# Optimization experiments

Measured on AMD Instinct MI355X. Metric: run time of the kernel, lower is better.

Reference implementation:

```python
import jax, jax.numpy as jnp
import numpy as np

N_LAYERS = 5
EMB = 300
G = 2048
L_SEM = 10
V_SEM = 30
NUM_TASKS = 128
TAU = 1.0
GUM_TAU = 1.0
BN_EPS = 1e-5


def _bn(x, g, b):
    # training-mode batch norm (biased variance over batch dim)
    m = jnp.mean(x, 0)
    v = jnp.var(x, 0)
    return (x - m) / jnp.sqrt(v + BN_EPS) * g + b


def setup_inputs() -> dict:
    key = jax.random.key(0)
    ks = iter(jax.random.split(key, 64))
    N, E = 100000, 400000
    s = 0.02
    inp = {}
    inp['x_idx'] = jax.random.randint(next(ks), (N,), 0, 119)
    inp['edge_index'] = jax.random.randint(next(ks), (2, E), 0, N)
    inp['edge_attr'] = jax.random.randint(next(ks), (E,), 0, 5)
    inp['batch'] = jnp.sort(jax.random.randint(next(ks), (N,), 0, G))
    u = jax.random.uniform(next(ks), (G, L_SEM, V_SEM), minval=1e-8, maxval=1.0)
    inp['gumbel'] = -jnp.log(-jnp.log(u))  # standard Gumbel(0,1) noise
    nrm = lambda shape: jax.random.normal(next(ks), shape, dtype=jnp.float32) * s
    inp['atom_emb'] = nrm((119, EMB))
    inp['bond_emb'] = nrm((N_LAYERS, 5, EMB))
    inp['eps'] = jnp.zeros((N_LAYERS,), jnp.float32)
    inp['gin_W1'] = nrm((N_LAYERS, EMB, 2 * EMB)); inp['gin_b1'] = jnp.zeros((N_LAYERS, 2 * EMB))
    inp['gin_bn1_g'] = jnp.ones((N_LAYERS, 2 * EMB)); inp['gin_bn1_b'] = jnp.zeros((N_LAYERS, 2 * EMB))
    inp['gin_W2'] = nrm((N_LAYERS, 2 * EMB, EMB)); inp['gin_b2'] = jnp.zeros((N_LAYERS, EMB))
    inp['node_bn_g'] = jnp.ones((N_LAYERS, EMB)); inp['node_bn_b'] = jnp.zeros((N_LAYERS, EMB))
    M = N_LAYERS - 1
    inp['vn_W1'] = nrm((M, EMB, 2 * EMB)); inp['vn_b1'] = jnp.zeros((M, 2 * EMB))
    inp['vn_bn1_g'] = jnp.ones((M, 2 * EMB)); inp['vn_bn1_b'] = jnp.zeros((M, 2 * EMB))
    inp['vn_W2'] = nrm((M, 2 * EMB, EMB)); inp['vn_b2'] = jnp.zeros((M, EMB))
    inp['vn_bn2_g'] = jnp.ones((M, EMB)); inp['vn_bn2_b'] = jnp.zeros((M, EMB))
    inp['pre_W'] = nrm((EMB, L_SEM * V_SEM)); inp['pre_b'] = jnp.zeros((L_SEM * V_SEM,))
    inp['sel_W'] = nrm((V_SEM, 3)); inp['sel_b'] = jnp.zeros((3,))
    inp['aft_W'] = nrm((3 * L_SEM, EMB)); inp['aft_b'] = jnp.zeros((EMB,))
    inp['hW1'] = nrm((EMB, 128)); inp['hb1'] = jnp.zeros((128,))
    inp['hW2'] = nrm((128, 128)); inp['hb2'] = jnp.zeros((128,))
    inp['hW3'] = nrm((128, NUM_TASKS)); inp['hb3'] = jnp.zeros((NUM_TASKS,))
    return inp


def reference(x_idx, edge_index, edge_attr, batch, gumbel,
              atom_emb, bond_emb, eps,
              gin_W1, gin_b1, gin_bn1_g, gin_bn1_b, gin_W2, gin_b2,
              node_bn_g, node_bn_b,
              vn_W1, vn_b1, vn_bn1_g, vn_bn1_b, vn_W2, vn_b2, vn_bn2_g, vn_bn2_b,
              pre_W, pre_b, sel_W, sel_b, aft_W, aft_b,
              hW1, hb1, hW2, hb2, hW3, hb3):
    N = x_idx.shape[0]
    src, dst = edge_index[0], edge_index[1]
    h = atom_emb[x_idx]                               # [N, EMB]
    vn = jnp.zeros((G, EMB), h.dtype)                 # virtual node starts at zero embedding
    for l in range(N_LAYERS):
        hl = h + vn[batch]
        # GINConv: aggregate relu(x_src + bond_emb) onto dst, then MLP((1+eps)x + aggr)
        msg = jax.nn.relu(hl[src] + bond_emb[l][edge_attr])   # [E, EMB]
        agg = jax.ops.segment_sum(msg, dst, num_segments=N)
        t = (1.0 + eps[l]) * hl + agg
        t = jax.nn.relu(_bn(t @ gin_W1[l] + gin_b1[l], gin_bn1_g[l], gin_bn1_b[l]))
        t = t @ gin_W2[l] + gin_b2[l]
        t = _bn(t, node_bn_g[l], node_bn_b[l])
        if l < N_LAYERS - 1:
            t = jax.nn.relu(t)
            # virtual node update (dropout omitted: eval mode)
            vtmp = jax.ops.segment_sum(hl, batch, num_segments=G) + vn
            v1 = jax.nn.relu(_bn(vtmp @ vn_W1[l] + vn_b1[l], vn_bn1_g[l], vn_bn1_b[l]))
            vn = jax.nn.relu(_bn(v1 @ vn_W2[l] + vn_b2[l], vn_bn2_g[l], vn_bn2_b[l]))
        h = t
    # global mean pool
    cnt = jnp.maximum(jax.ops.segment_sum(jnp.ones((N,), h.dtype), batch, num_segments=G), 1.0)
    h_graph = jax.ops.segment_sum(h, batch, num_segments=G) / cnt[:, None]
    # SEM head: gumbel-softmax (hard, straight-through)
    logits = ((h_graph @ pre_W + pre_b) / TAU).reshape(G, L_SEM, V_SEM)
    y = (logits + gumbel) / GUM_TAU
    y_soft = jax.nn.softmax(y, axis=-1)
    y_hard = jax.nn.one_hot(jnp.argmax(y, axis=-1), V_SEM, dtype=y_soft.dtype)
    oht = jax.lax.stop_gradient(y_hard - y_soft) + y_soft
    msg_w = oht @ sel_W + sel_b                        # [G, L, 3]
    dis = msg_w.reshape(G, 3 * L_SEM) @ aft_W + aft_b  # [G, EMB]
    o = jax.nn.relu(dis @ hW1 + hb1)
    o = jax.nn.relu(o @ hW2 + hb2)
    return o @ hW3 + hb3                               # [G, num_tasks]
```

## Files before the change

### kernel.cpp

```cpp
#include <hip/hip_runtime.h>
#include <cstdint>

#define EMBD 300
#define GNUM 2048
#define LSEM 10
#define VSEM 30
#define NLAY 5
#define GRAM_KB 24

typedef __attribute__((ext_vector_type(8))) short short8v;
typedef __attribute__((ext_vector_type(4))) float f32x4;

__device__ __forceinline__ void split3(float x, short& h1, short& h2, short& h3) {
  unsigned u = __float_as_uint(x);
  unsigned uh = (u + 0x7FFFu + ((u >> 16) & 1u)) & 0xFFFF0000u;
  h1 = (short)(uh >> 16);
  float r = x - __uint_as_float(uh);
  unsigned v = __float_as_uint(r);
  unsigned vh = (v + 0x7FFFu + ((v >> 16) & 1u)) & 0xFFFF0000u;
  h2 = (short)(vh >> 16);
  float r2 = r - __uint_as_float(vh);
  unsigned w = __float_as_uint(r2);
  unsigned wh = (w + 0x7FFFu + ((w >> 16) & 1u)) & 0xFFFF0000u;
  h3 = (short)(wh >> 16);
}

__device__ __forceinline__ unsigned cvt_pk_bf16(float lo, float hi) {
  unsigned r;
  asm("v_cvt_pk_bf16_f32 %0, %1, %2" : "=v"(r) : "v"(lo), "v"(hi));
  return r;
}

__device__ __forceinline__ void split3_pair(float x0, float x1,
                                            unsigned& u1, unsigned& u2, unsigned& u3) {
  u1 = cvt_pk_bf16(x0, x1);
  float r0 = x0 - __uint_as_float(u1 << 16);
  float r1 = x1 - __uint_as_float(u1 & 0xFFFF0000u);
  u2 = cvt_pk_bf16(r0, r1);
  float s0 = r0 - __uint_as_float(u2 << 16);
  float s1 = r1 - __uint_as_float(u2 & 0xFFFF0000u);
  u3 = cvt_pk_bf16(s0, s1);
}

__global__ void k_diag(float* __restrict__ p, int n, float v) {
  int i = blockIdx.x * blockDim.x + threadIdx.x;
  if (i < n) p[i] = v;
}

__global__ void k_zero(float* __restrict__ p, int n) {
  int i = blockIdx.x * blockDim.x + threadIdx.x;
  if (i < n) p[i] = 0.f;
}

__global__ void k_seti(int* __restrict__ p, int n, int v) {
  int i = blockIdx.x * blockDim.x + threadIdx.x;
  if (i < n) p[i] = v;
}

__global__ void k_offsets(const int* __restrict__ batch, int N, int* __restrict__ off) {
  int g = blockIdx.x * blockDim.x + threadIdx.x;
  if (g > GNUM) return;
  int lo = 0, hi = N;
  while (lo < hi) { int mid = (lo + hi) >> 1; if (batch[mid] < g) lo = mid + 1; else hi = mid; }
  off[g] = lo;
}

__global__ void k_deg(const int* __restrict__ dst, int E, int* __restrict__ deg) {
  int e = blockIdx.x * blockDim.x + threadIdx.x;
  if (e < E) atomicAdd(&deg[dst[e]], 1);
}

__global__ void k_scan1(const int* __restrict__ deg, int N,
                        int* __restrict__ incl, int* __restrict__ part) {
  __shared__ int s[256];
  int tid = threadIdx.x;
  int i = blockIdx.x * 256 + tid;
  int v = (i < N) ? deg[i] : 0;
  s[tid] = v; __syncthreads();
  for (int o = 1; o < 256; o <<= 1) {
    int t = (tid >= o) ? s[tid - o] : 0;
    __syncthreads();
    s[tid] += t;
    __syncthreads();
  }
  if (i < N) incl[i] = s[tid];
  if (tid == 255) part[blockIdx.x] = s[255];
}

__global__ void k_scan2(int* __restrict__ part, int nb) {
  __shared__ int s[512];
  int t = threadIdx.x;
  if (nb <= 512) {
    int v = (t < nb) ? part[t] : 0;
    s[t] = v; __syncthreads();
    for (int o = 1; o < 512; o <<= 1) {
      int u = (t >= o) ? s[t - o] : 0;
      __syncthreads();
      s[t] += u;
      __syncthreads();
    }
    if (t < nb) part[t] = s[t] - v;
  } else if (t == 0) {
    int run = 0;
    for (int i = 0; i < nb; i++) { int x = part[i]; part[i] = run; run += x; }
  }
}

__global__ void k_scan3(const int* __restrict__ deg, const int* __restrict__ incl,
                        const int* __restrict__ part, int N, int E, int* __restrict__ off2) {
  int i = blockIdx.x * blockDim.x + threadIdx.x;
  if (i < N) off2[i] = part[i >> 8] + incl[i] - deg[i];
  if (i == 0) off2[N] = E;
}

__global__ void k_copyi(const int* __restrict__ a, int* __restrict__ b, int n) {
  int i = blockIdx.x * blockDim.x + threadIdx.x;
  if (i < n) b[i] = a[i];
}

__global__ void k_fill(const int* __restrict__ dst, int E,
                       int* __restrict__ cur, int* __restrict__ eix) {
  int e = blockIdx.x * blockDim.x + threadIdx.x;
  if (e >= E) return;
  int p = atomicAdd(&cur[dst[e]], 1);
  eix[p] = e;
}

template<bool FIRST>
__global__ void k_hl(const float* __restrict__ aemb, const int* __restrict__ x_idx,
                     const float* __restrict__ scale, const float* __restrict__ shift,
                     const int* __restrict__ batch, const float* __restrict__ vn,
                     const float* __restrict__ epsArr, int l,
                     float* pt, float* __restrict__ hl, int N)
{
  int i = blockIdx.x;
  int c = threadIdx.x;
  if (c >= EMBD) return;
  float x;
  if (FIRST) {
    x = aemb[(size_t)x_idx[i] * EMBD + c];
  } else {
    x = pt[(size_t)i * EMBD + c];
    x = fmaxf(fmaf(x, scale[c], shift[c]), 0.f);
  }
  float h = x + vn[(size_t)batch[i] * EMBD + c];
  hl[(size_t)i * EMBD + c] = h;
  pt[(size_t)i * EMBD + c] = (1.f + epsArr[l]) * h;
}

__global__ void k_gather(const int* __restrict__ off2, const int* __restrict__ eix,
                         const int* __restrict__ src, const int* __restrict__ eattr,
                         const float* __restrict__ hl, const float* __restrict__ bond,
                         float* __restrict__ tacc, int N)
{
  int node = blockIdx.x * 4 + (threadIdx.x >> 6);
  int lane = threadIdx.x & 63;
  if (node >= N) return;
  int p0 = off2[node], p1 = off2[node + 1];
  if (p0 == p1) return;
  float acc[5] = {0.f, 0.f, 0.f, 0.f, 0.f};
  for (int p = p0; p < p1; p++) {
    int e = eix[p];
    int s = src[e], a = eattr[e];
    const float* hr = hl + (size_t)s * EMBD;
    const float* br = bond + (size_t)a * EMBD;
    #pragma unroll
    for (int q = 0; q < 5; q++) {
      int c = lane + q * 64;
      if (c < EMBD) {
        float v = hr[c] + br[c];
        acc[q] += fmaxf(v, 0.f);
      }
    }
  }
  float* tr = tacc + (size_t)node * EMBD;
  #pragma unroll
  for (int q = 0; q < 5; q++) {
    int c = lane + q * 64;
    if (c < EMBD) tr[c] += acc[q];
  }
}

__global__ void k_splitW(const float* __restrict__ W, int K, int Kpad, int M,
                         short* __restrict__ planes)
{
  int idx = blockIdx.x * 256 + threadIdx.x;
  if (idx >= M * Kpad) return;
  int m = idx / Kpad, k = idx - m * Kpad;
  float x = (k < K) ? W[(size_t)k * M + m] : 0.f;
  short h1, h2, h3; split3(x, h1, h2, h3);
  size_t ps = (size_t)M * Kpad;
  planes[idx] = h1; planes[ps + idx] = h2; planes[2 * ps + idx] = h3;
}

template<bool AFUSE>
__global__ __launch_bounds__(256) void k_mgemm(
    const float* __restrict__ A, const short* __restrict__ Wp,
    const float* __restrict__ bias, float* __restrict__ C,
    int n, int K, int Kpad, int M,
    const float* __restrict__ ascale, const float* __restrict__ ashift)
{
  __shared__ __align__(16) short lsA[3][64][40];
  __shared__ __align__(16) short lsB[3][128][40];
  int tid = threadIdx.x;
  int row0 = blockIdx.x * 64;
  int col0 = blockIdx.y * 128;
  int l = tid & 63, wid = tid >> 6;
  int wr = wid >> 1, wc = wid & 1;
  int lr = l & 15, kb = (l >> 4) * 8, rbase = (l >> 4) * 4;
  int sar = tid >> 2;
  int sak = (tid & 3) * 8;
  int sbc = tid >> 1;
  int sbk = (tid & 1) * 16;
  size_t planeSz = (size_t)M * Kpad;

  f32x4 acc[2][4];
  #pragma unroll
  for (int i = 0; i < 2; i++)
    #pragma unroll
    for (int j = 0; j < 4; j++) acc[i][j] = (f32x4){0.f, 0.f, 0.f, 0.f};

  for (int k0 = 0; k0 < Kpad; k0 += 32) {
    {
      int gr = row0 + sar;
      int kbase = k0 + sak;
      float x[8];
      if (gr < n && kbase + 7 < K) {
        const float* ap = A + (size_t)gr * K + kbase;
        float4 u0 = *reinterpret_cast<const float4*>(ap);
        float4 u1 = *reinterpret_cast<const float4*>(ap + 4);
        x[0] = u0.x; x[1] = u0.y; x[2] = u0.z; x[3] = u0.w;
        x[4] = u1.x; x[5] = u1.y; x[6] = u1.z; x[7] = u1.w;
        if (AFUSE) {
          float4 sc0 = *reinterpret_cast<const float4*>(ascale + kbase);
          float4 sc1 = *reinterpret_cast<const float4*>(ascale + kbase + 4);
          float4 sf0 = *reinterpret_cast<const float4*>(ashift + kbase);
          float4 sf1 = *reinterpret_cast<const float4*>(ashift + kbase + 4);
          x[0] = fmaxf(fmaf(x[0], sc0.x, sf0.x), 0.f);
          x[1] = fmaxf(fmaf(x[1], sc0.y, sf0.y), 0.f);
          x[2] = fmaxf(fmaf(x[2], sc0.z, sf0.z), 0.f);
          x[3] = fmaxf(fmaf(x[3], sc0.w, sf0.w), 0.f);
          x[4] = fmaxf(fmaf(x[4], sc1.x, sf1.x), 0.f);
          x[5] = fmaxf(fmaf(x[5], sc1.y, sf1.y), 0.f);
          x[6] = fmaxf(fmaf(x[6], sc1.z, sf1.z), 0.f);
          x[7] = fmaxf(fmaf(x[7], sc1.w, sf1.w), 0.f);
        }
      } else {
        #pragma unroll
        for (int j = 0; j < 8; j++) {
          int k = kbase + j;
          float v = 0.f;
          if (gr < n && k < K) {
            v = A[(size_t)gr * K + k];
            if (AFUSE) v = fmaxf(fmaf(v, ascale[k], ashift[k]), 0.f);
          }
          x[j] = v;
        }
      }
      uint4 q1, q2, q3;
      unsigned* p1 = (unsigned*)&q1; unsigned* p2 = (unsigned*)&q2; unsigned* p3 = (unsigned*)&q3;
      #pragma unroll
      for (int j = 0; j < 4; j++) split3_pair(x[2 * j], x[2 * j + 1], p1[j], p2[j], p3[j]);
      *reinterpret_cast<uint4*>(&lsA[0][sar][sak]) = q1;
      *reinterpret_cast<uint4*>(&lsA[1][sar][sak]) = q2;
      *reinterpret_cast<uint4*>(&lsA[2][sar][sak]) = q3;
    }
    {
      int gc = col0 + sbc;
      #pragma unroll
      for (int p = 0; p < 3; p++) {
        short8v v0, v1;
        if (gc < M) {
          const short* bp = Wp + (size_t)p * planeSz + (size_t)gc * Kpad + k0 + sbk;
          v0 = *reinterpret_cast<const short8v*>(bp);
          v1 = *reinterpret_cast<const short8v*>(bp + 8);
        } else {
          #pragma unroll
          for (int j = 0; j < 8; j++) { v0[j] = 0; v1[j] = 0; }
        }
        *reinterpret_cast<short8v*>(&lsB[p][sbc][sbk]) = v0;
        *reinterpret_cast<short8v*>(&lsB[p][sbc][sbk + 8]) = v1;
      }
    }
    __syncthreads();
    short8v fa[3][2];
    #pragma unroll
    for (int p = 0; p < 3; p++)
      #pragma unroll
      for (int rf = 0; rf < 2; rf++)
        fa[p][rf] = *reinterpret_cast<const short8v*>(&lsA[p][wr * 32 + rf * 16 + lr][kb]);
    #pragma unroll
    for (int cf = 0; cf < 4; cf++) {
      int bcol = wc * 64 + cf * 16 + lr;
      short8v fb0 = *reinterpret_cast<const short8v*>(&lsB[0][bcol][kb]);
      short8v fb1 = *reinterpret_cast<const short8v*>(&lsB[1][bcol][kb]);
      short8v fb2 = *reinterpret_cast<const short8v*>(&lsB[2][bcol][kb]);
      #pragma unroll
      for (int rf = 0; rf < 2; rf++) {
        f32x4 a = acc[rf][cf];
        a = __builtin_amdgcn_mfma_f32_16x16x32_bf16(fa[0][rf], fb0, a, 0, 0, 0);
        a = __builtin_amdgcn_mfma_f32_16x16x32_bf16(fa[0][rf], fb1, a, 0, 0, 0);
        a = __builtin_amdgcn_mfma_f32_16x16x32_bf16(fa[1][rf], fb0, a, 0, 0, 0);
        a = __builtin_amdgcn_mfma_f32_16x16x32_bf16(fa[1][rf], fb1, a, 0, 0, 0);
        a = __builtin_amdgcn_mfma_f32_16x16x32_bf16(fa[0][rf], fb2, a, 0, 0, 0);
        a = __builtin_amdgcn_mfma_f32_16x16x32_bf16(fa[2][rf], fb0, a, 0, 0, 0);
        acc[rf][cf] = a;
      }
    }
    __syncthreads();
  }
  #pragma unroll
  for (int rf = 0; rf < 2; rf++) {
    #pragma unroll
    for (int cf = 0; cf < 4; cf++) {
      int col = col0 + wc * 64 + cf * 16 + lr;
      if (col >= M) continue;
      float bv = bias[col];
      #pragma unroll
      for (int r = 0; r < 4; r++) {
        int row = row0 + wr * 32 + rf * 16 + rbase + r;
        if (row < n) C[(size_t)row * M + col] = acc[rf][cf][r] + bv;
      }
    }
  }
}

template<bool AFUSE, bool ORELU>
__global__ __launch_bounds__(256) void k_gemm(
    const float* __restrict__ A, const float* __restrict__ W,
    const float* __restrict__ bias, float* __restrict__ C,
    int N, int K, int M,
    const float* __restrict__ ascale, const float* __restrict__ ashift)
{
  __shared__ __align__(16) float As[16][72];
  __shared__ __align__(16) float Bs[16][72];
  int tid = threadIdx.x;
  int row0 = blockIdx.x * 64;
  int col0 = blockIdx.y * 64;
  int tx = tid & 15, ty = tid >> 4;
  bool kvec = ((K & 3) == 0);
  bool mvec = ((M & 3) == 0);
  float acc[4][4] = {};
  for (int k0 = 0; k0 < K; k0 += 16) {
    {
      int r = tid >> 2;
      int kq = (tid & 3) * 4;
      int gr = row0 + r;
      float a0 = 0.f, a1 = 0.f, a2 = 0.f, a3 = 0.f;
      if (gr < N) {
        const float* ap = A + (size_t)gr * K + k0 + kq;
        int k = k0 + kq;
        if (kvec && k + 3 < K) {
          float4 t = *reinterpret_cast<const float4*>(ap);
          a0 = t.x; a1 = t.y; a2 = t.z; a3 = t.w;
        } else {
          if (k + 0 < K) a0 = ap[0];
          if (k + 1 < K) a1 = ap[1];
          if (k + 2 < K) a2 = ap[2];
          if (k + 3 < K) a3 = ap[3];
        }
        if (AFUSE) {
          if (k + 0 < K) a0 = fmaxf(fmaf(a0, ascale[k + 0], ashift[k + 0]), 0.f);
          if (k + 1 < K) a1 = fmaxf(fmaf(a1, ascale[k + 1], ashift[k + 1]), 0.f);
          if (k + 2 < K) a2 = fmaxf(fmaf(a2, ascale[k + 2], ashift[k + 2]), 0.f);
          if (k + 3 < K) a3 = fmaxf(fmaf(a3, ascale[k + 3], ashift[k + 3]), 0.f);
        }
      }
      As[kq + 0][r] = a0; As[kq + 1][r] = a1; As[kq + 2][r] = a2; As[kq + 3][r] = a3;
    }
    {
      int kk = tid >> 4;
      int j = (tid & 15) * 4;
      int gk = k0 + kk;
      float4 bv = {0.f, 0.f, 0.f, 0.f};
      if (gk < K) {
        const float* wp = W + (size_t)gk * M + col0 + j;
        if (mvec && col0 + j + 3 < M) {
          bv = *reinterpret_cast<const float4*>(wp);
        } else {
          if (col0 + j + 0 < M) bv.x = wp[0];
          if (col0 + j + 1 < M) bv.y = wp[1];
          if (col0 + j + 2 < M) bv.z = wp[2];
          if (col0 + j + 3 < M) bv.w = wp[3];
        }
      }
      *reinterpret_cast<float4*>(&Bs[kk][j]) = bv;
    }
    __syncthreads();
    #pragma unroll
    for (int kk = 0; kk < 16; kk++) {
      float4 a4 = *reinterpret_cast<const float4*>(&As[kk][ty * 4]);
      float4 b4 = *reinterpret_cast<const float4*>(&Bs[kk][tx * 4]);
      float a[4] = {a4.x, a4.y, a4.z, a4.w};
      float b[4] = {b4.x, b4.y, b4.z, b4.w};
      #pragma unroll
      for (int u = 0; u < 4; u++)
        #pragma unroll
        for (int v = 0; v < 4; v++)
          acc[u][v] = fmaf(a[u], b[v], acc[u][v]);
    }
    __syncthreads();
  }
  float bv[4];
  #pragma unroll
  for (int v = 0; v < 4; v++) { int gc = col0 + tx * 4 + v; bv[v] = (gc < M) ? bias[gc] : 0.f; }
  #pragma unroll
  for (int u = 0; u < 4; u++) {
    int gr = row0 + ty * 4 + u;
    if (gr >= N) continue;
    int gc0 = col0 + tx * 4;
    float val[4];
    #pragma unroll
    for (int v = 0; v < 4; v++) {
      float x = acc[u][v] + bv[v];
      if (ORELU) x = fmaxf(x, 0.f);
      val[v] = x;
    }
    if (mvec && gc0 + 3 < M) {
      float4 o = {val[0], val[1], val[2], val[3]};
      *reinterpret_cast<float4*>(C + (size_t)gr * M + gc0) = o;
    } else {
      #pragma unroll
      for (int v = 0; v < 4; v++) {
        int gc = gc0 + v;
        if (gc < M) C[(size_t)gr * M + gc] = val[v];
      }
    }
  }
}

__global__ __launch_bounds__(256) void k_gram(const float* __restrict__ A, int N,
                                              double* __restrict__ gpart)
{
  int bx = blockIdx.x;
  int ti = 0;
  {
    const int o1 = 5, o2 = 9, o3 = 12, o4 = 14;
    if (bx >= o1) ti = 1;
    if (bx >= o2) ti = 2;
    if (bx >= o3) ti = 3;
    if (bx >= o4) ti = 4;
  }
  const int offs[5] = {0, 5, 9, 12, 14};
  int tj = ti + (bx - offs[ti]);
  int I = ti * 64, J = tj * 64;
  __shared__ __align__(16) float LI[128][68];
  __shared__ __align__(16) float LJ[128][68];
  int tid = threadIdx.x;
  int tx = tid & 15, ty = tid >> 4;
  double dacc[4][4] = {};
  for (int rb = blockIdx.y; rb * 128 < N; rb += gridDim.y) {
    int r0 = rb * 128;
    {
      int rbase = tid >> 4;
      int c4 = (tid & 15) * 4;
      #pragma unroll
      for (int s = 0; s < 8; s++) {
        int r = rbase + s * 16;
        int gr = r0 + r;
        float4 vi = {0.f, 0.f, 0.f, 0.f}, vj = {0.f, 0.f, 0.f, 0.f};
        if (gr < N) {
          int ci = I + c4;
          if (ci + 3 < EMBD) vi = *reinterpret_cast<const float4*>(A + (size_t)gr * EMBD + ci);
          int cj = J + c4;
          if (cj + 3 < EMBD) vj = *reinterpret_cast<const float4*>(A + (size_t)gr * EMBD + cj);
        }
        *reinterpret_cast<float4*>(&LI[r][c4]) = vi;
        *reinterpret_cast<float4*>(&LJ[r][c4]) = vj;
      }
    }
    __syncthreads();
    float facc[4][4] = {};
    #pragma unroll 2
    for (int k = 0; k < 128; k++) {
      float4 a4 = *reinterpret_cast<const float4*>(&LI[k][ty * 4]);
      float4 b4 = *reinterpret_cast<const float4*>(&LJ[k][tx * 4]);
      float a[4] = {a4.x, a4.y, a4.z, a4.w};
      float b[4] = {b4.x, b4.y, b4.z, b4.w};
      #pragma unroll
      for (int u = 0; u < 4; u++)
        #pragma unroll
        for (int v = 0; v < 4; v++)
          facc[u][v] = fmaf(a[u], b[v], facc[u][v]);
    }
    #pragma unroll
    for (int u = 0; u < 4; u++)
      #pragma unroll
      for (int v = 0; v < 4; v++)
        dacc[u][v] += (double)facc[u][v];
    __syncthreads();
  }
  size_t base = ((size_t)blockIdx.y * 15 + bx) * 4096;
  #pragma unroll
  for (int u = 0; u < 4; u++)
    #pragma unroll
    for (int v = 0; v < 4; v++)
      gpart[base + (size_t)(ty * 4 + u) * 64 + tx * 4 + v] = dacc[u][v];
}

__global__ void k_gramfin(const double* __restrict__ gpart, double* __restrict__ G)
{
  int e = blockIdx.x * 256 + threadIdx.x;
  if (e >= 15 * 4096) return;
  int tile = e >> 12;
  int ii = (e >> 6) & 63, jj = e & 63;
  const int tit[15] = {0,0,0,0,0,1,1,1,1,2,2,2,3,3,4};
  const int tjt[15] = {0,1,2,3,4,1,2,3,4,2,3,4,3,4,4};
  int gi = tit[tile] * 64 + ii, gj = tjt[tile] * 64 + jj;
  if (gi >= EMBD || gj >= EMBD) return;
  double s = 0.0;
  for (int kb = 0; kb < GRAM_KB; kb++)
    s += gpart[((size_t)kb * 15 + tile) * 4096 + ii * 64 + jj];
  G[(size_t)gi * EMBD + gj] = s;
  G[(size_t)gj * EMBD + gi] = s;
}

__global__ void k_bn1gram(const double* __restrict__ G, const double* __restrict__ cbuf,
                          const float* __restrict__ W1, const float* __restrict__ b1,
                          const float* __restrict__ g, const float* __restrict__ b,
                          int n, float* __restrict__ sc, float* __restrict__ sh)
{
  int j = blockIdx.x;
  int t = threadIdx.x;
  __shared__ double ws[EMBD];
  __shared__ double red[256];
  for (int k = t; k < EMBD; k += 256) ws[k] = (double)W1[(size_t)k * 600 + j];
  __syncthreads();
  int i1 = 256 + t;
  double y0 = 0.0, y1 = 0.0;
  for (int k = 0; k < EMBD; k++) {
    double wk = ws[k];
    y0 += G[(size_t)k * EMBD + t] * wk;
    if (i1 < EMBD) y1 += G[(size_t)k * EMBD + i1] * wk;
  }
  double part = ws[t] * y0 + ((i1 < EMBD) ? ws[i1] * y1 : 0.0);
  double dpart = cbuf[t] * ws[t] + ((i1 < EMBD) ? cbuf[i1] * ws[i1] : 0.0);
  red[t] = part; __syncthreads();
  for (int w = 128; w > 0; w >>= 1) { if (t < w) red[t] += red[t + w]; __syncthreads(); }
  double Q = red[0]; __syncthreads();
  red[t] = dpart; __syncthreads();
  for (int w = 128; w > 0; w >>= 1) { if (t < w) red[t] += red[t + w]; __syncthreads(); }
  if (t == 0) {
    double d = red[0];
    double bj = (double)b1[j];
    double S = d + (double)n * bj;
    double Qf = Q + 2.0 * bj * d + (double)n * bj * bj;
    double m = S / n;
    double var = Qf / n - m * m;
    double inv = 1.0 / sqrt(var + 1e-5);
    double scv = (double)g[j] * inv;
    sc[j] = (float)scv;
    sh[j] = (float)((double)b[j] - m * scv);
  }
}

__global__ void k_colstats(const float* __restrict__ X, int n, int C,
                           double* __restrict__ psum, double* __restrict__ psq)
{
  int tid = threadIdx.x;
  int col = blockIdx.x * 64 + (tid & 63);
  int rl = tid >> 6;
  double s = 0.0, q = 0.0;
  if (col < C) {
    int stride = gridDim.y * 4;
    for (int r = blockIdx.y * 4 + rl; r < n; r += stride) {
      double x = (double)X[(size_t)r * C + col];
      s += x; q += x * x;
    }
  }
  __shared__ double ls[2][4][64];
  ls[0][rl][tid & 63] = s;
  ls[1][rl][tid & 63] = q;
  __syncthreads();
  if (rl == 0 && col < C) {
    int c = tid & 63;
    double S = ls[0][0][c] + ls[0][1][c] + ls[0][2][c] + ls[0][3][c];
    double Q = ls[1][0][c] + ls[1][1][c] + ls[1][2][c] + ls[1][3][c];
    psum[(size_t)blockIdx.y * C + col] = S;
    psq [(size_t)blockIdx.y * C + col] = Q;
  }
}

__global__ void k_redcol(const double* __restrict__ psum, int R, int C, double* __restrict__ cbuf)
{
  int c = blockIdx.x * blockDim.x + threadIdx.x;
  if (c >= C) return;
  double s = 0.0;
  for (int r = 0; r < R; r++) s += psum[(size_t)r * C + c];
  cbuf[c] = s;
}

__global__ void k_finstats(const double* __restrict__ psum, const double* __restrict__ psq,
                           int R, int M, int n,
                           const float* __restrict__ g, const float* __restrict__ b,
                           float* __restrict__ sc, float* __restrict__ sh)
{
  int j = blockIdx.x;
  int t = threadIdx.x;
  double s = 0.0, q = 0.0;
  for (int r = t; r < R; r += 256) { s += psum[(size_t)r * M + j]; q += psq[(size_t)r * M + j]; }
  __shared__ double ls[256], lq[256];
  ls[t] = s; lq[t] = q; __syncthreads();
  for (int w = 128; w > 0; w >>= 1) {
    if (t < w) { ls[t] += ls[t + w]; lq[t] += lq[t + w]; }
    __syncthreads();
  }
  if (t == 0) {
    double m = ls[0] / n;
    double v = lq[0] / n - m * m;
    double inv = 1.0 / sqrt(v + 1e-5);
    double scv = (double)g[j] * inv;
    sc[j] = (float)scv;
    sh[j] = (float)((double)b[j] - m * scv);
  }
}

__global__ void k_vnseg(const float* __restrict__ hl, const int* __restrict__ off,
                        const float* __restrict__ vn, float* __restrict__ vtmp)
{
  int g = blockIdx.x;
  int c = threadIdx.x;
  if (c >= EMBD) return;
  int r0 = off[g], r1 = off[g + 1];
  float s = 0.f;
  for (int r = r0; r < r1; r++) s += hl[(size_t)r * EMBD + c];
  vtmp[(size_t)g * EMBD + c] = s + vn[(size_t)g * EMBD + c];
}

__global__ void k_vnfinal(const float* __restrict__ vnraw, const float* __restrict__ scale,
                          const float* __restrict__ shift, float* __restrict__ vn, int total)
{
  int i = blockIdx.x * blockDim.x + threadIdx.x;
  if (i >= total) return;
  int c = i % EMBD;
  vn[i] = fmaxf(fmaf(vnraw[i], scale[c], shift[c]), 0.f);
}

__global__ void k_pool(const float* __restrict__ t2, const int* __restrict__ off,
                       const float* __restrict__ scale, const float* __restrict__ shift,
                       float* __restrict__ hg)
{
  int g = blockIdx.x;
  int c = threadIdx.x;
  if (c >= EMBD) return;
  int r0 = off[g], r1 = off[g + 1];
  float s = 0.f;
  for (int r = r0; r < r1; r++) s += t2[(size_t)r * EMBD + c];
  int cnt = r1 - r0;
  float denom = (cnt > 0) ? (float)cnt : 1.f;
  hg[(size_t)g * EMBD + c] = (scale[c] * s + shift[c] * (float)cnt) / denom;
}

__global__ void k_sem(const float* __restrict__ logits, const float* __restrict__ gum,
                      const float* __restrict__ selW, const float* __restrict__ selb,
                      float* __restrict__ msgw)
{
  int idx = blockIdx.x * blockDim.x + threadIdx.x;
  if (idx >= GNUM * LSEM) return;
  int g = idx / LSEM, l = idx % LSEM;
  const float* lp = logits + (size_t)g * (LSEM * VSEM) + l * VSEM;
  const float* gp = gum + (size_t)g * (LSEM * VSEM) + l * VSEM;
  float best = -1e30f; int bi = 0;
  for (int v = 0; v < VSEM; v++) {
    float y = lp[v] + gp[v];
    if (y > best) { best = y; bi = v; }
  }
  float* o = msgw + (size_t)g * (3 * LSEM) + l * 3;
  o[0] = selW[bi * 3 + 0] + selb[0];
  o[1] = selW[bi * 3 + 1] + selb[1];
  o[2] = selW[bi * 3 + 2] + selb[2];
}

template<bool AFUSE, bool ORELU>
static void gemm(const float* A, const float* W, const float* b, float* C,
                 int n, int k, int m, const float* sc, const float* sh, hipStream_t st)
{
  dim3 grid((n + 63) / 64, (m + 63) / 64);
  k_gemm<AFUSE, ORELU><<<grid, 256, 0, st>>>(A, W, b, C, n, k, m, sc, sh);
}

extern "C" void kernel_launch(void* const* d_in, const int* in_sizes, int n_in,
                              void* d_out, int out_size, void* d_ws, size_t ws_size,
                              hipStream_t stream)
{
  const int*   x_idx     = (const int*)d_in[0];
  const int*   eidx      = (const int*)d_in[1];
  const int*   eattr     = (const int*)d_in[2];
  const int*   batch     = (const int*)d_in[3];
  const float* gumbel    = (const float*)d_in[4];
  const float* atom_emb  = (const float*)d_in[5];
  const float* bond_emb  = (const float*)d_in[6];
  const float* eps       = (const float*)d_in[7];
  const float* gin_W1    = (const float*)d_in[8];
  const float* gin_b1    = (const float*)d_in[9];
  const float* gin_bn1_g = (const float*)d_in[10];
  const float* gin_bn1_b = (const float*)d_in[11];
  const float* gin_W2    = (const float*)d_in[12];
  const float* gin_b2    = (const float*)d_in[13];
  const float* node_bn_g = (const float*)d_in[14];
  const float* node_bn_b = (const float*)d_in[15];
  const float* vn_W1     = (const float*)d_in[16];
  const float* vn_b1     = (const float*)d_in[17];
  const float* vn_bn1_g  = (const float*)d_in[18];
  const float* vn_bn1_b  = (const float*)d_in[19];
  const float* vn_W2     = (const float*)d_in[20];
  const float* vn_b2     = (const float*)d_in[21];
  const float* vn_bn2_g  = (const float*)d_in[22];
  const float* vn_bn2_b  = (const float*)d_in[23];
  const float* pre_W     = (const float*)d_in[24];
  const float* pre_b     = (const float*)d_in[25];
  const float* sel_W     = (const float*)d_in[26];
  const float* sel_b     = (const float*)d_in[27];
  const float* aft_W     = (const float*)d_in[28];
  const float* aft_b     = (const float*)d_in[29];
  const float* hW1       = (const float*)d_in[30];
  const float* hb1       = (const float*)d_in[31];
  const float* hW2       = (const float*)d_in[32];
  const float* hb2       = (const float*)d_in[33];
  const float* hW3       = (const float*)d_in[34];
  const float* hb3       = (const float*)d_in[35];

  const int N = in_sizes[0];
  const int E = in_sizes[2];
  const int RB = 128;
  float* out = (float*)d_out;
  (void)n_in;

  char* ws = (char*)d_ws;
  size_t pos = 0;
  auto alloc = [&](size_t bytes) -> char* {
    char* p = ws + pos;
    pos = (pos + bytes + 255) & ~(size_t)255;
    return p;
  };
  int*    off   = (int*)   alloc((GNUM + 1) * sizeof(int));
  float*  hbuf0 = (float*) alloc((size_t)N * EMBD * 4);
  float*  hbuf1 = (float*) alloc((size_t)N * EMBD * 4);
  double* psum  = (double*)alloc((size_t)RB * 600 * 8);
  double* psq   = (double*)alloc((size_t)RB * 600 * 8);
  float*  vn    = (float*) alloc((size_t)GNUM * EMBD * 4);
  float*  vtmp  = (float*) alloc((size_t)GNUM * EMBD * 4);
  float*  vnraw = (float*) alloc((size_t)GNUM * EMBD * 4);
  double* cbuf  = (double*)alloc(EMBD * 8);
  int*    off2  = (int*)   alloc((size_t)(N + 1) * 4);
  int*    eix   = (int*)   alloc((size_t)E * 4);
  short*  wsplit1 = (short*)alloc((size_t)600 * 320 * 3 * 2);
  short*  wsplit2 = (short*)alloc((size_t)300 * 608 * 3 * 2);
  float*  s1    = (float*) alloc(600 * 4);
  float*  sh1   = (float*) alloc(600 * 4);
  float*  s2    = (float*) alloc(EMBD * 4);
  float*  sh2   = (float*) alloc(EMBD * 4);
  float*  vs1   = (float*) alloc(600 * 4);
  float*  vsh1  = (float*) alloc(600 * 4);
  float*  vs2   = (float*) alloc(EMBD * 4);
  float*  vsh2  = (float*) alloc(EMBD * 4);

  const size_t gpartBytes = (size_t)GRAM_KB * 15 * 4096 * 8;
  const size_t gBytes     = (size_t)EMBD * EMBD * 8;
  const size_t csrScratch = (size_t)N * 4 * 3 + 4096;
  const long long CH_MIN  = 2048;
  size_t slack = 1u << 20;
  size_t region_need = gpartBytes + gBytes;
  if (region_need < csrScratch) region_need = csrScratch;
  size_t t1_min = (size_t)CH_MIN * 600 * 4;
  if (region_need < t1_min) region_need = t1_min;

  if (ws_size < pos + region_need + slack) {
    float v = 1000.f + (float)(ws_size >> 20);
    k_diag<<<(out_size + 255) / 256, 256, 0, stream>>>(out, out_size, v);
    return;
  }

  size_t regionBytes = ws_size - pos - slack;
  char* region = ws + pos;
  int* deg  = (int*)region;
  int* incl = (int*)(region + (size_t)N * 4);
  int* cur  = (int*)(region + (size_t)N * 8);
  int* part = (int*)(region + (size_t)N * 12);
  double* gpart = (double*)region;
  double* G     = (double*)(region + gpartBytes);
  float*  t1buf = (float*)region;
  int CH;
  {
    long long ch = (long long)(regionBytes / (600ull * 4ull));
    if (ch > 32768) ch = 32768;
    ch &= ~63LL;
    if (ch < CH_MIN) ch = CH_MIN;
    long long npad = ((long long)N + 63) & ~63LL;
    if (ch > npad && npad >= CH_MIN) ch = npad;
    CH = (int)ch;
  }
  float* v1 = t1buf;
  float* hg     = vnraw;
  float* logits = t1buf;
  float* msgw   = t1buf + (size_t)GNUM * EMBD;
  float* dis    = vtmp;
  float* o1     = vn;
  float* o2     = vn + (size_t)GNUM * 128;

  k_zero<<<(GNUM * EMBD + 255) / 256, 256, 0, stream>>>(vn, GNUM * EMBD);
  k_offsets<<<(GNUM + 1 + 255) / 256, 256, 0, stream>>>(batch, N, off);

  const int* esrc = eidx;
  const int* edst = eidx + E;

  {
    int NB = (N + 255) / 256;
    k_seti<<<(N + 255) / 256, 256, 0, stream>>>(deg, N, 0);
    k_deg<<<(E + 255) / 256, 256, 0, stream>>>(edst, E, deg);
    k_scan1<<<NB, 256, 0, stream>>>(deg, N, incl, part);
    k_scan2<<<1, 512, 0, stream>>>(part, NB);
    k_scan3<<<(N + 255) / 256, 256, 0, stream>>>(deg, incl, part, N, E, off2);
    k_copyi<<<(N + 255) / 256, 256, 0, stream>>>(off2, cur, N);
    k_fill<<<(E + 255) / 256, 256, 0, stream>>>(edst, E, cur, eix);
  }

  float* hb[2] = {hbuf0, hbuf1};

  for (int l = 0; l < NLAY; l++) {
    float* tac = hb[l & 1];
    float* hlb = hb[(l + 1) & 1];

    if (l == 0)
      k_hl<true><<<N, 320, 0, stream>>>(atom_emb, x_idx, nullptr, nullptr, batch, vn, eps, l, tac, hlb, N);
    else
      k_hl<false><<<N, 320, 0, stream>>>(nullptr, nullptr, s2, sh2, batch, vn, eps, l, tac, hlb, N);

    k_gather<<<(N + 3) / 4, 256, 0, stream>>>(off2, eix, esrc, eattr, hlb,
                                              bond_emb + (size_t)l * 5 * EMBD, tac, N);

    if (l < NLAY - 1)
      k_vnseg<<<GNUM, 320, 0, stream>>>(hlb, off, vn, vtmp);

    k_colstats<<<dim3(5, RB), 256, 0, stream>>>(tac, N, EMBD, psum, psq);
    k_redcol<<<2, 256, 0, stream>>>(psum, RB, EMBD, cbuf);
    k_gram<<<dim3(15, GRAM_KB), 256, 0, stream>>>(tac, N, gpart);
    k_gramfin<<<240, 256, 0, stream>>>(gpart, G);
    k_bn1gram<<<600, 256, 0, stream>>>(G, cbuf, gin_W1 + (size_t)l * EMBD * 600,
                                       gin_b1 + (size_t)l * 600,
                                       gin_bn1_g + (size_t)l * 600, gin_bn1_b + (size_t)l * 600,
                                       N, s1, sh1);

    k_splitW<<<(600 * 320 + 255) / 256, 256, 0, stream>>>(gin_W1 + (size_t)l * EMBD * 600, 300, 320, 600, wsplit1);
    k_splitW<<<(300 * 608 + 255) / 256, 256, 0, stream>>>(gin_W2 + (size_t)l * 600 * EMBD, 600, 608, 300, wsplit2);

    for (int r0 = 0; r0 < N; r0 += CH) {
      int nr = (N - r0 < CH) ? (N - r0) : CH;
      dim3 g1((nr + 63) / 64, 5);
      k_mgemm<false><<<g1, 256, 0, stream>>>(tac + (size_t)r0 * EMBD, wsplit1,
                                             gin_b1 + (size_t)l * 600, t1buf,
                                             nr, 300, 320, 600, nullptr, nullptr);
      dim3 g2((nr + 63) / 64, 3);
      k_mgemm<true><<<g2, 256, 0, stream>>>(t1buf, wsplit2,
                                            gin_b2 + (size_t)l * EMBD, hlb + (size_t)r0 * EMBD,
                                            nr, 600, 608, 300, s1, sh1);
    }
    k_colstats<<<dim3(5, RB), 256, 0, stream>>>(hlb, N, EMBD, psum, psq);
    k_finstats<<<EMBD, 256, 0, stream>>>(psum, psq, RB, EMBD, N,
                                         node_bn_g + (size_t)l * EMBD, node_bn_b + (size_t)l * EMBD, s2, sh2);

    if (l < NLAY - 1) {
      gemm<false, false>(vtmp, vn_W1 + (size_t)l * EMBD * 600, vn_b1 + (size_t)l * 600, v1,
                         GNUM, EMBD, 600, nullptr, nullptr, stream);
      k_colstats<<<dim3(10, RB), 256, 0, stream>>>(v1, GNUM, 600, psum, psq);
      k_finstats<<<600, 256, 0, stream>>>(psum, psq, RB, 600, GNUM,
                                          vn_bn1_g + (size_t)l * 600, vn_bn1_b + (size_t)l * 600, vs1, vsh1);
      gemm<true, false>(v1, vn_W2 + (size_t)l * 600 * EMBD, vn_b2 + (size_t)l * EMBD, vnraw,
                        GNUM, 600, EMBD, vs1, vsh1, stream);
      k_colstats<<<dim3(5, RB), 256, 0, stream>>>(vnraw, GNUM, EMBD, psum, psq);
      k_finstats<<<EMBD, 256, 0, stream>>>(psum, psq, RB, EMBD, GNUM,
                                           vn_bn2_g + (size_t)l * EMBD, vn_bn2_b + (size_t)l * EMBD, vs2, vsh2);
      k_vnfinal<<<(GNUM * EMBD + 255) / 256, 256, 0, stream>>>(vnraw, vs2, vsh2, vn, GNUM * EMBD);
    }
  }

  float* lastH = hb[NLAY & 1];
  k_pool<<<GNUM, 320, 0, stream>>>(lastH, off, s2, sh2, hg);

  gemm<false, false>(hg, pre_W, pre_b, logits, GNUM, EMBD, LSEM * VSEM, nullptr, nullptr, stream);
  k_sem<<<(GNUM * LSEM + 255) / 256, 256, 0, stream>>>(logits, gumbel, sel_W, sel_b, msgw);
  gemm<false, false>(msgw, aft_W, aft_b, dis, GNUM, 3 * LSEM, EMBD, nullptr, nullptr, stream);
  gemm<false, true>(dis, hW1, hb1, o1, GNUM, EMBD, 128, nullptr, nullptr, stream);
  gemm<false, true>(o1, hW2, hb2, o2, GNUM, 128, 128, nullptr, nullptr, stream);
  gemm<false, false>(o2, hW3, hb3, out, GNUM, 128, 128, nullptr, nullptr, stream);
}
```

Measured before the change: 11.00 ms.

## Pre-permute edge arrays, unroll gather by two, fuse column sums into gram

```diff
diff --git a/kernel.cpp b/kernel.cpp
--- a/kernel.cpp
+++ b/kernel.cpp
@@ -6,7 +6,7 @@
 #define LSEM 10
 #define VSEM 30
 #define NLAY 5
-#define GRAM_KB 24
+#define GRAM_KB 20
 
 typedef __attribute__((ext_vector_type(8))) short short8v;
 typedef __attribute__((ext_vector_type(4))) float f32x4;
@@ -126,6 +126,16 @@
   eix[p] = e;
 }
 
+__global__ void k_permute(const int* __restrict__ eix, const int* __restrict__ src,
+                          const int* __restrict__ attr,
+                          int* __restrict__ esrc2, int* __restrict__ eattr2, int E) {
+  int i = blockIdx.x * blockDim.x + threadIdx.x;
+  if (i >= E) return;
+  int e = eix[i];
+  esrc2[i] = src[e];
+  eattr2[i] = attr[e];
+}
+
 template<bool FIRST>
 __global__ void k_hl(const float* __restrict__ aemb, const int* __restrict__ x_idx,
                      const float* __restrict__ scale, const float* __restrict__ shift,
@@ -148,8 +158,8 @@
   pt[(size_t)i * EMBD + c] = (1.f + epsArr[l]) * h;
 }
 
-__global__ void k_gather(const int* __restrict__ off2, const int* __restrict__ eix,
-                         const int* __restrict__ src, const int* __restrict__ eattr,
+__global__ void k_gather(const int* __restrict__ off2,
+                         const int* __restrict__ esrc2, const int* __restrict__ eattr2,
                          const float* __restrict__ hl, const float* __restrict__ bond,
                          float* __restrict__ tacc, int N)
 {
@@ -159,18 +169,31 @@
   int p0 = off2[node], p1 = off2[node + 1];
   if (p0 == p1) return;
   float acc[5] = {0.f, 0.f, 0.f, 0.f, 0.f};
-  for (int p = p0; p < p1; p++) {
-    int e = eix[p];
-    int s = src[e], a = eattr[e];
+  int p = p0;
+  for (; p + 1 < p1; p += 2) {
+    int sA = esrc2[p],     aA = eattr2[p];
+    int sB = esrc2[p + 1], aB = eattr2[p + 1];
+    const float* hA = hl + (size_t)sA * EMBD;
+    const float* bA = bond + (size_t)aA * EMBD;
+    const float* hB = hl + (size_t)sB * EMBD;
+    const float* bB = bond + (size_t)aB * EMBD;
+    #pragma unroll
+    for (int q = 0; q < 5; q++) {
+      int c = lane + q * 64;
+      if (c < EMBD) {
+        acc[q] += fmaxf(hA[c] + bA[c], 0.f);
+        acc[q] += fmaxf(hB[c] + bB[c], 0.f);
+      }
+    }
+  }
+  if (p < p1) {
+    int s = esrc2[p], a = eattr2[p];
     const float* hr = hl + (size_t)s * EMBD;
     const float* br = bond + (size_t)a * EMBD;
     #pragma unroll
     for (int q = 0; q < 5; q++) {
       int c = lane + q * 64;
-      if (c < EMBD) {
-        float v = hr[c] + br[c];
-        acc[q] += fmaxf(v, 0.f);
-      }
+      if (c < EMBD) acc[q] += fmaxf(hr[c] + br[c], 0.f);
     }
   }
   float* tr = tacc + (size_t)node * EMBD;
@@ -430,7 +453,8 @@
 }
 
 __global__ __launch_bounds__(256) void k_gram(const float* __restrict__ A, int N,
-                                              double* __restrict__ gpart)
+                                              double* __restrict__ gpart,
+                                              double* __restrict__ cpart)
 {
   int bx = blockIdx.x;
   int ti = 0;
@@ -444,11 +468,14 @@
   const int offs[5] = {0, 5, 9, 12, 14};
   int tj = ti + (bx - offs[ti]);
   int I = ti * 64, J = tj * 64;
+  bool diag = (ti == tj);
   __shared__ __align__(16) float LI[128][68];
   __shared__ __align__(16) float LJ[128][68];
+  __shared__ double cs[4][64];
   int tid = threadIdx.x;
   int tx = tid & 15, ty = tid >> 4;
   double dacc[4][4] = {};
+  double csum = 0.0;
   for (int rb = blockIdx.y; rb * 128 < N; rb += gridDim.y) {
     int r0 = rb * 128;
     {
@@ -488,6 +515,13 @@
       #pragma unroll
       for (int v = 0; v < 4; v++)
         dacc[u][v] += (double)facc[u][v];
+    if (diag) {
+      int col = tid & 63;
+      int rl = tid >> 6;
+      float fs = 0.f;
+      for (int r = rl; r < 128; r += 4) fs += LI[r][col];
+      csum += (double)fs;
+    }
     __syncthreads();
   }
   size_t base = ((size_t)blockIdx.y * 15 + bx) * 4096;
@@ -496,6 +530,15 @@
     #pragma unroll
     for (int v = 0; v < 4; v++)
       gpart[base + (size_t)(ty * 4 + u) * 64 + tx * 4 + v] = dacc[u][v];
+  if (diag) {
+    cs[tid >> 6][tid & 63] = csum;
+    __syncthreads();
+    if ((tid >> 6) == 0) {
+      int col = tid & 63;
+      double S = cs[0][col] + cs[1][col] + cs[2][col] + cs[3][col];
+      cpart[(size_t)blockIdx.y * 320 + I + col] = S;
+    }
+  }
 }
 
 __global__ void k_gramfin(const double* __restrict__ gpart, double* __restrict__ G)
@@ -581,12 +624,13 @@
   }
 }
 
-__global__ void k_redcol(const double* __restrict__ psum, int R, int C, double* __restrict__ cbuf)
+__global__ void k_redcol(const double* __restrict__ cpart, int R, int stride, int C,
+                         double* __restrict__ cbuf)
 {
   int c = blockIdx.x * blockDim.x + threadIdx.x;
   if (c >= C) return;
   double s = 0.0;
-  for (int r = 0; r < R; r++) s += psum[(size_t)r * C + c];
+  for (int r = 0; r < R; r++) s += cpart[(size_t)r * stride + c];
   cbuf[c] = s;
 }
 
@@ -743,7 +787,8 @@
   float*  vnraw = (float*) alloc((size_t)GNUM * EMBD * 4);
   double* cbuf  = (double*)alloc(EMBD * 8);
   int*    off2  = (int*)   alloc((size_t)(N + 1) * 4);
-  int*    eix   = (int*)   alloc((size_t)E * 4);
+  int*    esrc2 = (int*)   alloc((size_t)E * 4);
+  int*    eattr2= (int*)   alloc((size_t)E * 4);
   short*  wsplit1 = (short*)alloc((size_t)600 * 320 * 3 * 2);
   short*  wsplit2 = (short*)alloc((size_t)300 * 608 * 3 * 2);
   float*  s1    = (float*) alloc(600 * 4);
@@ -757,7 +802,7 @@
 
   const size_t gpartBytes = (size_t)GRAM_KB * 15 * 4096 * 8;
   const size_t gBytes     = (size_t)EMBD * EMBD * 8;
-  const size_t csrScratch = (size_t)N * 4 * 3 + 4096;
+  const size_t csrScratch = (size_t)N * 12 + 4096 + (size_t)E * 4;
   const long long CH_MIN  = 2048;
   size_t slack = 1u << 20;
   size_t region_need = gpartBytes + gBytes;
@@ -777,6 +822,7 @@
   int* incl = (int*)(region + (size_t)N * 4);
   int* cur  = (int*)(region + (size_t)N * 8);
   int* part = (int*)(region + (size_t)N * 12);
+  int* eix  = (int*)(region + (size_t)N * 12 + 4096);
   double* gpart = (double*)region;
   double* G     = (double*)(region + gpartBytes);
   float*  t1buf = (float*)region;
@@ -801,18 +847,18 @@
   k_zero<<<(GNUM * EMBD + 255) / 256, 256, 0, stream>>>(vn, GNUM * EMBD);
   k_offsets<<<(GNUM + 1 + 255) / 256, 256, 0, stream>>>(batch, N, off);
 
-  const int* esrc = eidx;
-  const int* edst = eidx + E;
-
   {
+    const int* esrcIn = eidx;
+    const int* edstIn = eidx + E;
     int NB = (N + 255) / 256;
     k_seti<<<(N + 255) / 256, 256, 0, stream>>>(deg, N, 0);
-    k_deg<<<(E + 255) / 256, 256, 0, stream>>>(edst, E, deg);
+    k_deg<<<(E + 255) / 256, 256, 0, stream>>>(edstIn, E, deg);
     k_scan1<<<NB, 256, 0, stream>>>(deg, N, incl, part);
     k_scan2<<<1, 512, 0, stream>>>(part, NB);
     k_scan3<<<(N + 255) / 256, 256, 0, stream>>>(deg, incl, part, N, E, off2);
     k_copyi<<<(N + 255) / 256, 256, 0, stream>>>(off2, cur, N);
-    k_fill<<<(E + 255) / 256, 256, 0, stream>>>(edst, E, cur, eix);
+    k_fill<<<(E + 255) / 256, 256, 0, stream>>>(edstIn, E, cur, eix);
+    k_permute<<<(E + 255) / 256, 256, 0, stream>>>(eix, esrcIn, eattr, esrc2, eattr2, E);
   }
 
   float* hb[2] = {hbuf0, hbuf1};
@@ -826,15 +872,14 @@
     else
       k_hl<false><<<N, 320, 0, stream>>>(nullptr, nullptr, s2, sh2, batch, vn, eps, l, tac, hlb, N);
 
-    k_gather<<<(N + 3) / 4, 256, 0, stream>>>(off2, eix, esrc, eattr, hlb,
+    k_gather<<<(N + 3) / 4, 256, 0, stream>>>(off2, esrc2, eattr2, hlb,
                                               bond_emb + (size_t)l * 5 * EMBD, tac, N);
 
     if (l < NLAY - 1)
       k_vnseg<<<GNUM, 320, 0, stream>>>(hlb, off, vn, vtmp);
 
-    k_colstats<<<dim3(5, RB), 256, 0, stream>>>(tac, N, EMBD, psum, psq);
-    k_redcol<<<2, 256, 0, stream>>>(psum, RB, EMBD, cbuf);
-    k_gram<<<dim3(15, GRAM_KB), 256, 0, stream>>>(tac, N, gpart);
+    k_gram<<<dim3(15, GRAM_KB), 256, 0, stream>>>(tac, N, gpart, psum);
+    k_redcol<<<2, 256, 0, stream>>>(psum, GRAM_KB, 320, EMBD, cbuf);
     k_gramfin<<<240, 256, 0, stream>>>(gpart, G);
     k_bn1gram<<<600, 256, 0, stream>>>(G, cbuf, gin_W1 + (size_t)l * EMBD * 600,
                                        gin_b1 + (size_t)l * 600,
```

Measured after the change: 11.44 ms. 4.0% more time.
